# Performance work log

Hardware: AMD Instinct MI355X
Metric: run time of the kernel (lower is better)

The kernel has to match this reference:

```python
import jax, jax.numpy as jnp
import numpy as np

B, N, E = 4, 4096, 16384
D, A_DIM = 256, 64
T, HALF, STEPS, NTYPES = 16, 8, 3, 50


def setup_inputs() -> dict:
    key = jax.random.key(0)
    ks = jax.random.split(key, 16)
    s = 0.02  # small init so repeated DxD matmuls stay stable over 3 steps
    return {
        "annotation_id": jax.random.randint(ks[0], (B, N), 0, NTYPES),
        "src": jax.random.randint(ks[1], (B, E), 0, N),
        "dst": jax.random.randint(ks[2], (B, E), 0, N),
        "etype": jax.random.randint(ks[3], (B, E), 0, HALF),
        "edge_embed": jax.random.normal(ks[4], (T, D * D), jnp.float32) * s,
        "edge_bias": jax.random.normal(ks[5], (T, D), jnp.float32) * s,
        "type_embed": jax.random.normal(ks[6], (NTYPES, A_DIM), jnp.float32) * s,
        "Wr": jax.random.normal(ks[7], (D, 3 * D), jnp.float32) * s,
        "br": jnp.zeros((D,), jnp.float32),
        "Wz": jax.random.normal(ks[8], (D, 3 * D), jnp.float32) * s,
        "bz": jnp.zeros((D,), jnp.float32),
        "Wh": jax.random.normal(ks[9], (D, 3 * D), jnp.float32) * s,
        "bh": jnp.zeros((D,), jnp.float32),
        "Wa": jax.random.normal(ks[10], (1, D + A_DIM), jnp.float32) * s,
        "ba": jnp.zeros((1,), jnp.float32),
        "Wo": jax.random.normal(ks[11], (1, D + A_DIM), jnp.float32) * s,
        "bo": jnp.zeros((1,), jnp.float32),
    }


def reference(annotation_id, src, dst, etype, edge_embed, edge_bias, type_embed,
              Wr, br, Wz, bz, Wh, bh, Wa, ba, Wo, bo):
    # annotation: typeEmbed[id-1] if id>0 else zeros  -> [B, N, A_DIM]
    ann = jnp.where((annotation_id > 0)[..., None],
                    type_embed[jnp.clip(annotation_id - 1, 0, NTYPES - 1)],
                    jnp.zeros((), type_embed.dtype))
    # prop_state: annotation zero-padded to state_dim  -> [B, N, D]
    h = jnp.concatenate([ann, jnp.zeros((B, N, D - A_DIM), ann.dtype)], axis=-1)
    W = edge_embed.reshape(T, D, D)  # per-edge-type DxD matrices

    def step(h):
        # type-major projection: apply every edge-type matrix to every node state
        # P[b, t, n, :] = W[t] @ h[b, n]   -> [B, T, N, D]
        P = jnp.einsum('tij,bnj->btni', W, h)

        def per_graph(Pg, s_, d_, e_):
            # a_out[j]        += W[e] @ h[neighbour] + b[e]
            # a_in[neighbour] += W[e+HALF] @ h[j]   + b[e+HALF]
            m_out = Pg[e_, d_] + edge_bias[e_]            # [E, D]
            m_in = Pg[e_ + HALF, s_] + edge_bias[e_ + HALF]
            a_out = jnp.zeros((N, D), h.dtype).at[s_].add(m_out)
            a_in = jnp.zeros((N, D), h.dtype).at[d_].add(m_in)
            return a_in, a_out

        a_in, a_out = jax.vmap(per_graph)(P, src, dst, etype)
        # GRU-style propagator (dropout_rate = 0 -> identity)
        a = jnp.concatenate([a_in, a_out, h], axis=-1)    # [B, N, 3D]
        r = jax.nn.sigmoid(a @ Wr.T + br)
        z = jax.nn.sigmoid(a @ Wz.T + bz)
        h_hat = jnp.tanh(jnp.concatenate([a_in, a_out, r * h], axis=-1) @ Wh.T + bh)
        return (1.0 - z) * h + z * h_hat

    for _ in range(STEPS):
        h = step(h)

    join = jnp.concatenate([h, ann], axis=-1)             # [B, N, D+A]
    atten = jax.nn.sigmoid(join @ Wa.T + ba)              # [B, N, 1]
    ou = jnp.tanh(join @ Wo.T + bo)                       # [B, N, 1]
    w_sum = jnp.sum((atten * ou).reshape(-1, N), axis=1)  # [B]
    return jax.nn.sigmoid(w_sum)
```

## Files before the change

kernel.cpp:

```cpp
#include <hip/hip_runtime.h>
#include <cstdint>

#define BB 4
#define NN 4096
#define EE 16384
#define DD 256
#define ADIM 64
#define TT 16
#define HALFE 8
#define STEPS 3
#define OSTRIDE 4160
#define MAXTILES 1088
#define MAXM (MAXTILES * 128)

#define AS1 __attribute__((address_space(1)))
#define AS3 __attribute__((address_space(3)))

typedef __attribute__((ext_vector_type(8))) short short8;
typedef __attribute__((ext_vector_type(4))) float f32x4;

__device__ __forceinline__ float sigmoidf_(float x) { return 1.0f / (1.0f + __expf(-x)); }

__device__ __forceinline__ unsigned short f2bf(float x) {
    unsigned u = __float_as_uint(x);
    u += 0x7fffu + ((u >> 16) & 1u);
    return (unsigned short)(u >> 16);
}
__device__ __forceinline__ float bf2f(unsigned short b) {
    return __uint_as_float(((unsigned)b) << 16);
}

__global__ void prep_kernel(const int* __restrict__ ann_id, const float* __restrict__ type_embed,
                            const float* __restrict__ edge_embed, const float* __restrict__ Wr,
                            const float* __restrict__ Wz, const float* __restrict__ Wh,
                            float* __restrict__ ann, float* __restrict__ h,
                            unsigned short* __restrict__ hbf, unsigned short* __restrict__ Xbf,
                            unsigned short* __restrict__ W2bf, unsigned short* __restrict__ Wcatbf,
                            unsigned short* __restrict__ Whhbf, float* __restrict__ acc,
                            int* __restrict__ counts, int* __restrict__ c32,
                            int* __restrict__ map) {
    int bid = blockIdx.x, tid = threadIdx.x;
    if (bid < 4096) {
        if (bid < 128) counts[bid * 256 + tid] = 0;
        if (bid < 1024) map[bid * 256 + tid] = -1;
        if (bid == 0) { c32[tid] = 0; c32[256 + tid] = 0; c32[512 + tid] = 0; c32[768 + tid] = 0; }
        if (bid == 0 && tid < 16) acc[tid] = 0.f;
        int idx = bid * 256 + tid;
        int bn = idx >> 6, q = idx & 63;
        int id = ann_id[bn];
        float4 v = {0.f, 0.f, 0.f, 0.f};
        if (q < 16) {
            if (id > 0) v = ((const float4*)(type_embed + (size_t)(id - 1) * ADIM))[q];
            ((float4*)(ann + (size_t)bn * ADIM))[q] = v;
        }
        ((float4*)(h + (size_t)bn * DD))[q] = v;
        ushort4 o;
        o.x = f2bf(v.x); o.y = f2bf(v.y); o.z = f2bf(v.z); o.w = f2bf(v.w);
        ((ushort4*)(hbf + (size_t)bn * DD))[q] = o;
        ((ushort4*)(Xbf + (size_t)bn * 768 + 512))[q] = o;
    } else if (bid < 5120) {
        int idx = (bid - 4096) * 256 + tid;
        float4 v = ((const float4*)edge_embed)[idx];
        ushort4 o;
        o.x = f2bf(v.x); o.y = f2bf(v.y); o.z = f2bf(v.z); o.w = f2bf(v.w);
        ((ushort4*)W2bf)[idx] = o;
    } else if (bid < 7424) {
        int idx = (bid - 5120) * 256 + tid;
        int c = idx / 768, k = idx % 768;
        float v;
        if (c < 256)       v = Wr[c * 768 + k];
        else if (c < 512)  v = Wz[(c - 256) * 768 + k];
        else               v = (k < 512) ? Wh[(c - 512) * 768 + k] : 0.f;
        Wcatbf[idx] = f2bf(v);
    } else {
        int idx = (bid - 7424) * 256 + tid;
        int i = idx / 256, k = idx % 256;
        Whhbf[idx] = f2bf(Wh[i * 768 + 512 + k]);
    }
}

__global__ void claim_kernel(const int* __restrict__ src, const int* __restrict__ dst,
                             const int* __restrict__ et, int* __restrict__ counts,
                             int* __restrict__ c32, int* __restrict__ map) {
    __shared__ int cnt[64];
    __shared__ int bse[64];
    int tid = threadIdx.x;
    if (tid < 64) cnt[tid] = 0;
    __syncthreads();
    int idx = blockIdx.x * 256 + tid;
    int b = idx >> 14;
    int s = src[idx], d = dst[idx], t = et[idx];
    atomicAdd(&counts[(b * 2 + 0) * NN + s], 1);
    atomicAdd(&counts[(b * 2 + 1) * NN + d], 1);
    int bin0 = b * 16 + t;
    int bin1 = b * 16 + 8 + t;
    int k0 = (b << 16) | (t << 12) | d;
    int k1 = (b << 16) | ((t + 8) << 12) | s;
    bool w0 = (atomicCAS(&map[k0], -1, -2) == -1);
    bool w1 = (atomicCAS(&map[k1], -1, -2) == -1);
    int r0 = w0 ? atomicAdd(&cnt[bin0], 1) : 0;
    int r1 = w1 ? atomicAdd(&cnt[bin1], 1) : 0;
    __syncthreads();
    if (tid < 64) bse[tid] = cnt[tid] ? atomicAdd(&c32[tid * 16], cnt[tid]) : 0;
    __syncthreads();
    if (w0) map[k0] = bse[bin0] + r0;
    if (w1) map[k1] = bse[bin1] + r1;
}

__global__ __launch_bounds__(1024) void scan_kernel(const int* __restrict__ counts,
                                                    int* __restrict__ offs,
                                                    int* __restrict__ cursor) {
    __shared__ int lsum[1024];
    int t = threadIdx.x, seg = blockIdx.x;
    int4 v = ((const int4*)(counts + (size_t)seg * NN))[t];
    int s1 = v.x + v.y, s2 = s1 + v.z, s3 = s2 + v.w;
    lsum[t] = s3;
    __syncthreads();
    for (int off = 1; off < 1024; off <<= 1) {
        int tmp = (t >= off) ? lsum[t - off] : 0;
        __syncthreads();
        lsum[t] += tmp;
        __syncthreads();
    }
    int base = lsum[t] - s3;
    int* o = offs + (size_t)seg * OSTRIDE;
    o[4 * t] = base; o[4 * t + 1] = base + v.x; o[4 * t + 2] = base + s1; o[4 * t + 3] = base + s2;
    if (t == 1023) o[4096] = lsum[1023];
    int* c = cursor + (size_t)seg * NN;
    c[4 * t] = base; c[4 * t + 1] = base + v.x; c[4 * t + 2] = base + s1; c[4 * t + 3] = base + s2;
}

__global__ void scan2_kernel(const int* __restrict__ c32, int* __restrict__ type_cursor,
                             int* __restrict__ tile_type, int* __restrict__ idx2) {
    __shared__ int pad[64];
    int t = threadIdx.x;
    for (int k = t; k < MAXTILES; k += 64) tile_type[k] = -1;
    __syncthreads();
    int cnt = c32[t * 16];
    int padded = ((cnt + 127) >> 7) << 7;
    pad[t] = padded;
    __syncthreads();
    int off = 0;
    for (int k = 0; k < t; ++k) off += pad[k];
    type_cursor[t] = off;
    int t16 = t & 15;
    int tile0 = off >> 7;
    for (int k = 0; k < (padded >> 7); ++k) tile_type[tile0 + k] = t16;
    for (int r = off + cnt; r < off + padded; ++r) idx2[r] = 0;
}

__global__ void fill3_kernel(const int* __restrict__ src, const int* __restrict__ dst,
                             const int* __restrict__ et, const int* __restrict__ type_cursor,
                             int* __restrict__ node_cursor, int* __restrict__ entries,
                             int* __restrict__ idx2, const int* __restrict__ map) {
    int idx = blockIdx.x * 256 + threadIdx.x;
    int b = idx >> 14;
    int s = src[idx], d = dst[idx], t = et[idx];
    int k0 = (b << 16) | (t << 12) | d;
    int k1 = (b << 16) | ((t + 8) << 12) | s;
    int p0 = type_cursor[b * 16 + t] + map[k0];
    int p1 = type_cursor[b * 16 + t + 8] + map[k1];
    idx2[p0] = b * NN + d;
    idx2[p1] = b * NN + s;
    int q0 = atomicAdd(&node_cursor[(b * 2 + 0) * NN + s], 1);
    entries[(size_t)(b * 2 + 0) * EE + q0] = (p0 << 4) | t;
    int q1 = atomicAdd(&node_cursor[(b * 2 + 1) * NN + d], 1);
    entries[(size_t)(b * 2 + 1) * EE + q1] = (p1 << 4) | (t + 8);
}

#define COMP_128x64(cb)                                                                 \
    _Pragma("unroll")                                                                   \
    for (int kk = 0; kk < 2; ++kk) {                                                    \
        short8 af[4], bfv[2];                                                           \
        _Pragma("unroll")                                                               \
        for (int m = 0; m < 4; ++m) {                                                   \
            int R = wr * 64 + m * 16 + lr;                                              \
            af[m] = *(const short8*)((const char*)As + (cb) * 16384 + R * 128 + (((kk * 4 + hi) ^ rx) << 4)); \
        }                                                                               \
        _Pragma("unroll")                                                               \
        for (int n = 0; n < 2; ++n) {                                                   \
            int R = wc * 32 + n * 16 + lr;                                              \
            bfv[n] = *(const short8*)((const char*)Bs + (cb) * 8192 + R * 128 + (((kk * 4 + hi) ^ rx) << 4)); \
        }                                                                               \
        _Pragma("unroll")                                                               \
        for (int m = 0; m < 4; ++m)                                                     \
            _Pragma("unroll")                                                           \
            for (int n = 0; n < 2; ++n)                                                 \
                acc[m][n] = __builtin_amdgcn_mfma_f32_16x16x32_bf16(bfv[n], af[m], acc[m][n], 0, 0, 0); \
    }

#define PIPE_WAIT(NSTR)                                                                 \
    asm volatile("s_waitcnt vmcnt(" NSTR ")" ::: "memory");                             \
    __builtin_amdgcn_s_barrier();                                                       \
    __builtin_amdgcn_sched_barrier(0);

__global__ __launch_bounds__(256) void gemm_msgs(const unsigned short* __restrict__ A,
                                                 const unsigned short* __restrict__ W2,
                                                 const int* __restrict__ idx2,
                                                 const int* __restrict__ tile_type,
                                                 unsigned short* __restrict__ C) {
    __shared__ __align__(16) unsigned short As[2 * 128 * 64];
    __shared__ __align__(16) unsigned short Bs[2 * 64 * 64];
    const int bid = blockIdx.x;
    const int wg = (bid & 7) * (MAXTILES * 4 / 8) + (bid >> 3);
    const int by = wg >> 2, bx = wg & 3;
    const int t16 = tile_type[by];
    if (t16 < 0) return;
    const int r0 = by << 7, c0 = bx << 6;
    const int tid = threadIdx.x;
    const int wv = tid >> 6, lane = tid & 63;
    const int wr = wv >> 1, wc = wv & 1;
    const int lr = lane & 15, hi = lane >> 4, rx = lane & 7;
    const int strow = tid >> 3;
    const int scol = ((tid & 7) ^ ((tid >> 3) & 7)) << 3;
    int ar[4];
#pragma unroll
    for (int i = 0; i < 4; ++i) ar[i] = idx2[r0 + strow + i * 32];
    const unsigned short* Bg = W2 + (size_t)t16 * (DD * DD) + (size_t)(c0 + strow) * DD + scol;
    f32x4 acc[4][2] = {};
#define MS_STG(buf, kof)                                                                \
    { _Pragma("unroll")                                                                 \
      for (int i = 0; i < 4; ++i)                                                       \
          __builtin_amdgcn_global_load_lds(                                             \
              (const AS1 void*)(A + (size_t)ar[i] * DD + scol + (kof)),                 \
              (AS3 void*)((char*)As + (buf) * 16384 + wv * 1024 + i * 4096), 16, 0, 0); \
      __builtin_amdgcn_global_load_lds(                                                 \
          (const AS1 void*)(Bg + (kof)),                                                \
          (AS3 void*)((char*)Bs + (buf) * 8192 + wv * 1024), 16, 0, 0);                 \
      __builtin_amdgcn_global_load_lds(                                                 \
          (const AS1 void*)(Bg + (size_t)32 * DD + (kof)),                              \
          (AS3 void*)((char*)Bs + (buf) * 8192 + wv * 1024 + 4096), 16, 0, 0); }
    MS_STG(0, 0)
    for (int it = 0; it < 3; ++it) {
        MS_STG((it + 1) & 1, (it + 1) * 64)
        PIPE_WAIT("6")
        COMP_128x64(it & 1)
        __builtin_amdgcn_s_barrier();
    }
    PIPE_WAIT("0")
    COMP_128x64(1)
    const int erow = r0 + wr * 64 + lr;
    const int ecol = c0 + wc * 32 + (hi << 2);
#pragma unroll
    for (int m = 0; m < 4; ++m)
#pragma unroll
        for (int n = 0; n < 2; ++n) {
            ushort4 o;
            o.x = f2bf(acc[m][n][0]); o.y = f2bf(acc[m][n][1]);
            o.z = f2bf(acc[m][n][2]); o.w = f2bf(acc[m][n][3]);
            *(ushort4*)&C[(size_t)(erow + m * 16) * DD + ecol + n * 16] = o;
        }
}

__global__ __launch_bounds__(256) void gemm_rzu(const unsigned short* __restrict__ A,
                                                const unsigned short* __restrict__ Bt,
                                                const float* __restrict__ br,
                                                const float* __restrict__ bz,
                                                const float* __restrict__ h,
                                                unsigned short* __restrict__ RH,
                                                unsigned short* __restrict__ Zb,
                                                unsigned short* __restrict__ Ub) {
    __shared__ __align__(16) unsigned short As[2 * 128 * 64];
    __shared__ __align__(16) unsigned short Bs[2 * 64 * 64];
    const int bid = blockIdx.x;
    const int wg = (bid & 7) * 192 + (bid >> 3);
    const int bx = wg % 12, by = wg / 12;
    const int r0 = by << 7, c0 = bx << 6;
    const int tid = threadIdx.x;
    const int wv = tid >> 6, lane = tid & 63;
    const int wr = wv >> 1, wc = wv & 1;
    const int lr = lane & 15, hi = lane >> 4, rx = lane & 7;
    const int strow = tid >> 3;
    const int scol = ((tid & 7) ^ ((tid >> 3) & 7)) << 3;
    const unsigned short* Ag = A + (size_t)(r0 + strow) * 768 + scol;
    const unsigned short* Bg = Bt + (size_t)(c0 + strow) * 768 + scol;
    f32x4 acc[4][2] = {};
#define RZ_STG(buf, kof)                                                                \
    { _Pragma("unroll")                                                                 \
      for (int i = 0; i < 4; ++i)                                                       \
          __builtin_amdgcn_global_load_lds(                                             \
              (const AS1 void*)(Ag + (size_t)(i * 32) * 768 + (kof)),                   \
              (AS3 void*)((char*)As + (buf) * 16384 + wv * 1024 + i * 4096), 16, 0, 0); \
      __builtin_amdgcn_global_load_lds(                                                 \
          (const AS1 void*)(Bg + (kof)),                                                \
          (AS3 void*)((char*)Bs + (buf) * 8192 + wv * 1024), 16, 0, 0);                 \
      __builtin_amdgcn_global_load_lds(                                                 \
          (const AS1 void*)(Bg + (size_t)32 * 768 + (kof)),                             \
          (AS3 void*)((char*)Bs + (buf) * 8192 + wv * 1024 + 4096), 16, 0, 0); }
    RZ_STG(0, 0)
    for (int it = 0; it < 11; ++it) {
        RZ_STG((it + 1) & 1, (it + 1) * 64)
        PIPE_WAIT("6")
        COMP_128x64(it & 1)
        __builtin_amdgcn_s_barrier();
    }
    PIPE_WAIT("0")
    COMP_128x64(1)
    const int erow = r0 + wr * 64 + lr;
    const int ecol = c0 + wc * 32 + (hi << 2);
    const int region = c0 >> 8;
#pragma unroll
    for (int m = 0; m < 4; ++m)
#pragma unroll
        for (int n = 0; n < 2; ++n) {
            int gr = erow + m * 16;
            int gc = ecol + n * 16;
            f32x4 v = acc[m][n];
            if (region == 0) {
                float4 bb = *(const float4*)&br[gc];
                float4 hv = *(const float4*)&h[(size_t)gr * 256 + gc];
                ushort4 o;
                o.x = f2bf(sigmoidf_(v[0] + bb.x) * hv.x);
                o.y = f2bf(sigmoidf_(v[1] + bb.y) * hv.y);
                o.z = f2bf(sigmoidf_(v[2] + bb.z) * hv.z);
                o.w = f2bf(sigmoidf_(v[3] + bb.w) * hv.w);
                *(ushort4*)&RH[(size_t)gr * 256 + gc] = o;
            } else if (region == 1) {
                int c = gc - 256;
                float4 bb = *(const float4*)&bz[c];
                ushort4 o;
                o.x = f2bf(sigmoidf_(v[0] + bb.x));
                o.y = f2bf(sigmoidf_(v[1] + bb.y));
                o.z = f2bf(sigmoidf_(v[2] + bb.z));
                o.w = f2bf(sigmoidf_(v[3] + bb.w));
                *(ushort4*)&Zb[(size_t)gr * 256 + c] = o;
            } else {
                int c = gc - 512;
                ushort4 o;
                o.x = f2bf(v[0]); o.y = f2bf(v[1]); o.z = f2bf(v[2]); o.w = f2bf(v[3]);
                *(ushort4*)&Ub[(size_t)gr * 256 + c] = o;
            }
        }
}

__global__ __launch_bounds__(256) void gemm_hh(const unsigned short* __restrict__ A,
                                               const unsigned short* __restrict__ Bt,
                                               const unsigned short* __restrict__ Zb,
                                               const unsigned short* __restrict__ Ub,
                                               const float* __restrict__ bh,
                                               float* __restrict__ h,
                                               unsigned short* __restrict__ hbf,
                                               unsigned short* __restrict__ Xbf) {
    __shared__ __align__(16) unsigned short As[2 * 64 * 64];
    __shared__ __align__(16) unsigned short Bs[2 * 64 * 64];
    const int bid = blockIdx.x;
    const int wg = (bid & 7) * 128 + (bid >> 3);
    const int r0 = wg >> 2 << 6, c0 = (wg & 3) << 6;
    const int tid = threadIdx.x;
    const int wv = tid >> 6, lane = tid & 63;
    const int wr = wv >> 1, wc = wv & 1;
    const int lr = lane & 15, hi = lane >> 4, rx = lane & 7;
    const int srow = wv * 8 + (lane >> 3);
    const int scol = ((lane & 7) ^ (lane >> 3)) << 3;
    const unsigned short* Ag = A + (size_t)(r0 + srow) * 256 + scol;
    const unsigned short* Bg = Bt + (size_t)(c0 + srow) * 256 + scol;
    f32x4 acc[2][2] = {};
#define HH_STG(buf, kof)                                                                \
    { _Pragma("unroll")                                                                 \
      for (int i = 0; i < 2; ++i) {                                                     \
          __builtin_amdgcn_global_load_lds(                                             \
              (const AS1 void*)(Ag + (size_t)(i * 32) * 256 + (kof)),                   \
              (AS3 void*)((char*)As + (buf) * 8192 + wv * 1024 + i * 4096), 16, 0, 0);  \
          __builtin_amdgcn_global_load_lds(                                             \
              (const AS1 void*)(Bg + (size_t)(i * 32) * 256 + (kof)),                   \
              (AS3 void*)((char*)Bs + (buf) * 8192 + wv * 1024 + i * 4096), 16, 0, 0); } }
#define COMP_64x64(cb)                                                                  \
    _Pragma("unroll")                                                                   \
    for (int kk = 0; kk < 2; ++kk) {                                                    \
        short8 af[2], bfv[2];                                                           \
        _Pragma("unroll")                                                               \
        for (int m = 0; m < 2; ++m) {                                                   \
            int R = wr * 32 + m * 16 + lr;                                              \
            af[m] = *(const short8*)((const char*)As + (cb) * 8192 + R * 128 + (((kk * 4 + hi) ^ rx) << 4)); \
        }                                                                               \
        _Pragma("unroll")                                                               \
        for (int n = 0; n < 2; ++n) {                                                   \
            int R = wc * 32 + n * 16 + lr;                                              \
            bfv[n] = *(const short8*)((const char*)Bs + (cb) * 8192 + R * 128 + (((kk * 4 + hi) ^ rx) << 4)); \
        }                                                                               \
        _Pragma("unroll")                                                               \
        for (int m = 0; m < 2; ++m)                                                     \
            _Pragma("unroll")                                                           \
            for (int n = 0; n < 2; ++n)                                                 \
                acc[m][n] = __builtin_amdgcn_mfma_f32_16x16x32_bf16(bfv[n], af[m], acc[m][n], 0, 0, 0); \
    }
    HH_STG(0, 0)
    for (int it = 0; it < 3; ++it) {
        HH_STG((it + 1) & 1, (it + 1) * 64)
        PIPE_WAIT("4")
        COMP_64x64(it & 1)
        __builtin_amdgcn_s_barrier();
    }
    PIPE_WAIT("0")
    COMP_64x64(1)
    const int erow = r0 + wr * 32 + lr;
    const int ecol = c0 + wc * 32 + (hi << 2);
#pragma unroll
    for (int m = 0; m < 2; ++m)
#pragma unroll
        for (int n = 0; n < 2; ++n) {
            int gr = erow + m * 16;
            int gc = ecol + n * 16;
            size_t base = (size_t)gr * 256 + gc;
            f32x4 v = acc[m][n];
            float4 bb = *(const float4*)&bh[gc];
            float4 hv = *(const float4*)&h[base];
            ushort4 zp = *(const ushort4*)&Zb[base];
            ushort4 up = *(const ushort4*)&Ub[base];
            float4 hn;
            {
                float z = bf2f(zp.x); hn.x = (1.f - z) * hv.x + z * tanhf(bf2f(up.x) + v[0] + bb.x);
            }{
                float z = bf2f(zp.y); hn.y = (1.f - z) * hv.y + z * tanhf(bf2f(up.y) + v[1] + bb.y);
            }{
                float z = bf2f(zp.z); hn.z = (1.f - z) * hv.z + z * tanhf(bf2f(up.z) + v[2] + bb.z);
            }{
                float z = bf2f(zp.w); hn.w = (1.f - z) * hv.w + z * tanhf(bf2f(up.w) + v[3] + bb.w);
            }
            *(float4*)&h[base] = hn;
            ushort4 o;
            o.x = f2bf(hn.x); o.y = f2bf(hn.y); o.z = f2bf(hn.z); o.w = f2bf(hn.w);
            *(ushort4*)&hbf[base] = o;
            *(ushort4*)&Xbf[(size_t)gr * 768 + 512 + gc] = o;
        }
}

__global__ void gather2_kernel(const unsigned short* __restrict__ msgs,
                               const int* __restrict__ offs, const int* __restrict__ entries,
                               const float* __restrict__ bias, unsigned short* __restrict__ Xb) {
    int wv = threadIdx.x >> 6, lane = threadIdx.x & 63;
    int slot = blockIdx.x * 4 + wv;
    int b = slot >> 13;
    int dir = (slot >> 12) & 1;
    int node = slot & 4095;
    const int* o = offs + (size_t)(b * 2 + dir) * OSTRIDE;
    int beg = o[node], end = o[node + 1];
    const int* ent = entries + (size_t)(b * 2 + dir) * EE;
    const float4* bias4 = (const float4*)bias;
    float4 acc = {0.f, 0.f, 0.f, 0.f};
    for (int p = beg; p < end; ++p) {
        int e2 = ent[p];
        int row = e2 >> 4, t = e2 & 15;
        ushort4 pv = *(const ushort4*)(msgs + (size_t)row * DD + lane * 4);
        float4 bv = bias4[t * 64 + lane];
        acc.x += bf2f(pv.x) + bv.x;
        acc.y += bf2f(pv.y) + bv.y;
        acc.z += bf2f(pv.z) + bv.z;
        acc.w += bf2f(pv.w) + bv.w;
    }
    ushort4 o4;
    o4.x = f2bf(acc.x); o4.y = f2bf(acc.y); o4.z = f2bf(acc.z); o4.w = f2bf(acc.w);
    int colbase = (dir == 0 ? 256 : 0) + lane * 4;
    *(ushort4*)(Xb + ((size_t)b * NN + node) * 768 + colbase) = o4;
}

__global__ void final_reduce(const float* __restrict__ h, const float* __restrict__ ann,
                             const float* __restrict__ Wa, const float* __restrict__ ba,
                             const float* __restrict__ Wo, const float* __restrict__ bo,
                             float* __restrict__ acc) {
    int wv = threadIdx.x >> 6, lane = threadIdx.x & 63;
    int b = blockIdx.x >> 5;
    int nbase = (blockIdx.x & 31) * 128 + wv * 32;
    float4 wah = ((const float4*)Wa)[lane];
    float4 woh = ((const float4*)Wo)[lane];
    float4 waa = {0, 0, 0, 0}, woa = {0, 0, 0, 0};
    if (lane < 16) {
        waa = ((const float4*)(Wa + 256))[lane];
        woa = ((const float4*)(Wo + 256))[lane];
    }
    float bav = ba[0], bov = bo[0];
    float part = 0.f;
    for (int it = 0; it < 32; ++it) {
        int node = nbase + it;
        float4 hv = ((const float4*)(h + ((size_t)b * NN + node) * DD))[lane];
        float sa = hv.x * wah.x + hv.y * wah.y + hv.z * wah.z + hv.w * wah.w;
        float so = hv.x * woh.x + hv.y * woh.y + hv.z * woh.z + hv.w * woh.w;
        if (lane < 16) {
            float4 av = ((const float4*)(ann + ((size_t)b * NN + node) * ADIM))[lane];
            sa += av.x * waa.x + av.y * waa.y + av.z * waa.z + av.w * waa.w;
            so += av.x * woa.x + av.y * woa.y + av.z * woa.z + av.w * woa.w;
        }
        for (int off = 32; off; off >>= 1) {
            sa += __shfl_down(sa, off);
            so += __shfl_down(so, off);
        }
        if (lane == 0) part += sigmoidf_(sa + bav) * tanhf(so + bov);
    }
    if (lane == 0) atomicAdd(&acc[b], part);
}

__global__ void final_out(const float* __restrict__ acc, float* __restrict__ out) {
    int b = threadIdx.x;
    if (b < BB) out[b] = sigmoidf_(acc[b]);
}

extern "C" void kernel_launch(void* const* d_in, const int* in_sizes, int n_in,
                              void* d_out, int out_size, void* d_ws, size_t ws_size,
                              hipStream_t stream) {
    const int*   ann_id     = (const int*)d_in[0];
    const int*   src        = (const int*)d_in[1];
    const int*   dst        = (const int*)d_in[2];
    const int*   etype      = (const int*)d_in[3];
    const float* edge_embed = (const float*)d_in[4];
    const float* edge_bias  = (const float*)d_in[5];
    const float* type_embed = (const float*)d_in[6];
    const float* Wr = (const float*)d_in[7];
    const float* br = (const float*)d_in[8];
    const float* Wz = (const float*)d_in[9];
    const float* bz = (const float*)d_in[10];
    const float* Wh = (const float*)d_in[11];
    const float* bh = (const float*)d_in[12];
    const float* Wa = (const float*)d_in[13];
    const float* ba = (const float*)d_in[14];
    const float* Wo = (const float*)d_in[15];
    const float* bo = (const float*)d_in[16];
    float* out = (float*)d_out;

    char* base = (char*)d_ws;
    size_t off = 0;
    auto alloc = [&](size_t bytes) { char* p = base + off; off += (bytes + 255) & ~(size_t)255; return p; };
    float* ann  = (float*)alloc((size_t)BB * NN * ADIM * 4);
    float* h    = (float*)alloc((size_t)BB * NN * DD * 4);
    float* acc  = (float*)alloc(64);
    unsigned short* h_bf   = (unsigned short*)alloc((size_t)BB * NN * DD * 2);
    unsigned short* W2bf   = (unsigned short*)alloc((size_t)TT * DD * DD * 2);
    unsigned short* Wcatbf = (unsigned short*)alloc(768 * 768 * 2);
    unsigned short* Whhbf  = (unsigned short*)alloc(256 * 256 * 2);
    unsigned short* msgs   = (unsigned short*)alloc((size_t)MAXM * DD * 2);
    unsigned short* Xbf    = (unsigned short*)alloc((size_t)BB * NN * 768 * 2);
    unsigned short* RHbf   = (unsigned short*)alloc((size_t)BB * NN * DD * 2);
    unsigned short* Zb     = (unsigned short*)alloc((size_t)BB * NN * DD * 2);
    unsigned short* Ub     = (unsigned short*)alloc((size_t)BB * NN * DD * 2);
    int* counts  = (int*)alloc((size_t)BB * 2 * NN * 4);
    int* c32     = (int*)alloc(1024 * 4);
    int* cursor  = (int*)alloc((size_t)BB * 2 * NN * 4);
    int* offsets = (int*)alloc((size_t)BB * 2 * OSTRIDE * 4);
    int* entries = (int*)alloc((size_t)BB * 2 * EE * 4);
    int* tcur    = (int*)alloc(64 * 4);
    int* ttype   = (int*)alloc(MAXTILES * 4);
    int* idx2    = (int*)alloc((size_t)MAXM * 4);
    int* map     = (int*)alloc((size_t)262144 * 4);

    prep_kernel<<<dim3(7680), dim3(256), 0, stream>>>(
        ann_id, type_embed, edge_embed, Wr, Wz, Wh,
        ann, h, h_bf, Xbf, W2bf, Wcatbf, Whhbf, acc, counts, c32, map);
    claim_kernel<<<dim3((BB * EE) / 256), dim3(256), 0, stream>>>(
        src, dst, etype, counts, c32, map);
    scan_kernel<<<dim3(BB * 2), dim3(1024), 0, stream>>>(counts, offsets, cursor);
    scan2_kernel<<<dim3(1), dim3(64), 0, stream>>>(c32, tcur, ttype, idx2);
    fill3_kernel<<<dim3((BB * EE) / 256), dim3(256), 0, stream>>>(
        src, dst, etype, tcur, cursor, entries, idx2, map);

    for (int s = 0; s < STEPS; ++s) {
        gemm_msgs<<<dim3(MAXTILES * 4), dim3(256), 0, stream>>>(
            h_bf, W2bf, idx2, ttype, msgs);
        gather2_kernel<<<dim3(BB * 2 * NN / 4), dim3(256), 0, stream>>>(
            msgs, offsets, entries, edge_bias, Xbf);
        gemm_rzu<<<dim3(1536), dim3(256), 0, stream>>>(
            Xbf, Wcatbf, br, bz, h, RHbf, Zb, Ub);
        gemm_hh<<<dim3(1024), dim3(256), 0, stream>>>(
            RHbf, Whhbf, Zb, Ub, bh, h, h_bf, Xbf);
    }

    final_reduce<<<dim3(128), dim3(256), 0, stream>>>(h, ann, Wa, ba, Wo, bo, acc);
    final_out<<<dim3(1), dim3(64), 0, stream>>>(acc, out);
}
```

Measured before the change: 411.4 us.

## Widen gemm_msgs tile to full 256 output columns, drop double buffering

Each workgroup of the message GEMM now computes a 128x256 output tile (all D columns) instead of 128x64, so the gathered A rows are loaded once per row tile rather than four times. The grid shrinks to one block per row tile. The double-buffered pipelined staging is replaced with a single-buffered loop with __syncthreads around each K chunk, removing load/compute overlap. Accumulators grow to 32 MFMA tiles per wave, which raises register pressure and reduces parallelism.

```diff
diff --git a/kernel.cpp b/kernel.cpp
--- a/kernel.cpp
+++ b/kernel.cpp
@@ -199,14 +199,13 @@
                                                  const int* __restrict__ idx2,
                                                  const int* __restrict__ tile_type,
                                                  unsigned short* __restrict__ C) {
-    __shared__ __align__(16) unsigned short As[2 * 128 * 64];
-    __shared__ __align__(16) unsigned short Bs[2 * 64 * 64];
+    __shared__ __align__(16) unsigned short As[128 * 64];
+    __shared__ __align__(16) unsigned short Bs[256 * 64];
     const int bid = blockIdx.x;
-    const int wg = (bid & 7) * (MAXTILES * 4 / 8) + (bid >> 3);
-    const int by = wg >> 2, bx = wg & 3;
+    const int by = (bid & 7) * (MAXTILES / 8) + (bid >> 3);
     const int t16 = tile_type[by];
     if (t16 < 0) return;
-    const int r0 = by << 7, c0 = bx << 6;
+    const int r0 = by << 7;
     const int tid = threadIdx.x;
     const int wv = tid >> 6, lane = tid & 63;
     const int wr = wv >> 1, wc = wv & 1;
@@ -216,35 +215,47 @@
     int ar[4];
 #pragma unroll
     for (int i = 0; i < 4; ++i) ar[i] = idx2[r0 + strow + i * 32];
-    const unsigned short* Bg = W2 + (size_t)t16 * (DD * DD) + (size_t)(c0 + strow) * DD + scol;
-    f32x4 acc[4][2] = {};
-#define MS_STG(buf, kof)                                                                \
-    { _Pragma("unroll")                                                                 \
-      for (int i = 0; i < 4; ++i)                                                       \
-          __builtin_amdgcn_global_load_lds(                                             \
-              (const AS1 void*)(A + (size_t)ar[i] * DD + scol + (kof)),                 \
-              (AS3 void*)((char*)As + (buf) * 16384 + wv * 1024 + i * 4096), 16, 0, 0); \
-      __builtin_amdgcn_global_load_lds(                                                 \
-          (const AS1 void*)(Bg + (kof)),                                                \
-          (AS3 void*)((char*)Bs + (buf) * 8192 + wv * 1024), 16, 0, 0);                 \
-      __builtin_amdgcn_global_load_lds(                                                 \
-          (const AS1 void*)(Bg + (size_t)32 * DD + (kof)),                              \
-          (AS3 void*)((char*)Bs + (buf) * 8192 + wv * 1024 + 4096), 16, 0, 0); }
-    MS_STG(0, 0)
-    for (int it = 0; it < 3; ++it) {
-        MS_STG((it + 1) & 1, (it + 1) * 64)
-        PIPE_WAIT("6")
-        COMP_128x64(it & 1)
-        __builtin_amdgcn_s_barrier();
-    }
-    PIPE_WAIT("0")
-    COMP_128x64(1)
+    const unsigned short* Bg = W2 + (size_t)t16 * (DD * DD) + (size_t)strow * DD + scol;
+    f32x4 acc[4][8] = {};
+    for (int k0 = 0; k0 < DD; k0 += 64) {
+#pragma unroll
+        for (int i = 0; i < 4; ++i)
+            __builtin_amdgcn_global_load_lds(
+                (const AS1 void*)(A + (size_t)ar[i] * DD + scol + k0),
+                (AS3 void*)((char*)As + wv * 1024 + i * 4096), 16, 0, 0);
+#pragma unroll
+        for (int i = 0; i < 8; ++i)
+            __builtin_amdgcn_global_load_lds(
+                (const AS1 void*)(Bg + (size_t)(i * 32) * DD + k0),
+                (AS3 void*)((char*)Bs + wv * 1024 + i * 4096), 16, 0, 0);
+        __syncthreads();
+#pragma unroll
+        for (int kk = 0; kk < 2; ++kk) {
+            short8 af[4], bfv[8];
+#pragma unroll
+            for (int m = 0; m < 4; ++m) {
+                int R = wr * 64 + m * 16 + lr;
+                af[m] = *(const short8*)((const char*)As + R * 128 + (((kk * 4 + hi) ^ rx) << 4));
+            }
+#pragma unroll
+            for (int n = 0; n < 8; ++n) {
+                int R = wc * 128 + n * 16 + lr;
+                bfv[n] = *(const short8*)((const char*)Bs + R * 128 + (((kk * 4 + hi) ^ rx) << 4));
+            }
+#pragma unroll
+            for (int m = 0; m < 4; ++m)
+#pragma unroll
+                for (int n = 0; n < 8; ++n)
+                    acc[m][n] = __builtin_amdgcn_mfma_f32_16x16x32_bf16(bfv[n], af[m], acc[m][n], 0, 0, 0);
+        }
+        __syncthreads();
+    }
     const int erow = r0 + wr * 64 + lr;
-    const int ecol = c0 + wc * 32 + (hi << 2);
+    const int ecol = wc * 128 + (hi << 2);
 #pragma unroll
     for (int m = 0; m < 4; ++m)
 #pragma unroll
-        for (int n = 0; n < 2; ++n) {
+        for (int n = 0; n < 8; ++n) {
             ushort4 o;
             o.x = f2bf(acc[m][n][0]); o.y = f2bf(acc[m][n][1]);
             o.z = f2bf(acc[m][n][2]); o.w = f2bf(acc[m][n][3]);
@@ -552,7 +563,7 @@
         src, dst, etype, tcur, cursor, entries, idx2, map);
 
     for (int s = 0; s < STEPS; ++s) {
-        gemm_msgs<<<dim3(MAXTILES * 4), dim3(256), 0, stream>>>(
+        gemm_msgs<<<dim3(MAXTILES), dim3(256), 0, stream>>>(
             h_bf, W2bf, idx2, ttype, msgs);
         gather2_kernel<<<dim3(BB * 2 * NN / 4), dim3(256), 0, stream>>>(
             msgs, offsets, entries, edge_bias, Xbf);
```

New measurement: 471.7 us. +14.7%, slower.
